# Performance work log

Measured on AMD Instinct MI355X. Metric: run time of the kernel, lower is better.

The kernel has to match this reference:

```python
import jax, jax.numpy as jnp
import numpy as np

DEPTH = 6
INPUT_DIM = 512
HIDDEN = [128, 64]
OUT_DIM = 8
BATCH = 8192
NUM_LEAVES = 2 ** DEPTH            # 64
NUM_INTERNAL = 2 ** DEPTH - 1      # 63 routing Dense(1, sigmoid) nodes


def setup_inputs() -> dict:
    key = jax.random.key(0)
    ks = jax.random.split(key, 9)
    s = lambda fan_in: 1.0 / np.sqrt(fan_in)
    return {
        "x": jax.random.normal(ks[0], (BATCH, INPUT_DIM), dtype=jnp.float32),
        # routers: one Dense(input_dim -> 1) per internal node
        "router_W": jax.random.normal(ks[1], (NUM_INTERNAL, INPUT_DIM), dtype=jnp.float32) * s(INPUT_DIM),
        "router_b": jnp.zeros((NUM_INTERNAL,), dtype=jnp.float32),
        # leaf MLPs: Dense(512->128, relu) -> Dense(128->64, relu) -> Dense(64->8, linear), one per leaf
        "W1": jax.random.normal(ks[2], (NUM_LEAVES, INPUT_DIM, HIDDEN[0]), dtype=jnp.float32) * s(INPUT_DIM),
        "b1": jnp.zeros((NUM_LEAVES, HIDDEN[0]), dtype=jnp.float32),
        "W2": jax.random.normal(ks[3], (NUM_LEAVES, HIDDEN[0], HIDDEN[1]), dtype=jnp.float32) * s(HIDDEN[0]),
        "b2": jnp.zeros((NUM_LEAVES, HIDDEN[1]), dtype=jnp.float32),
        "W3": jax.random.normal(ks[4], (NUM_LEAVES, HIDDEN[1], OUT_DIM), dtype=jnp.float32) * s(HIDDEN[1]),
        "b3": jnp.zeros((NUM_LEAVES, OUT_DIM), dtype=jnp.float32),
    }


def reference(x, router_W, router_b, W1, b1, W2, b2, W3, b3):
    B = x.shape[0]
    depth = int(np.log2(router_W.shape[0] + 1))
    # All routing probabilities in one fused GEMM: [B, num_internal]
    route = jax.nn.sigmoid(jnp.einsum('bi,ni->bn', x, router_W) + router_b)
    # Soft routing down the tree: interleave left/right child probabilities per level.
    p = jnp.ones((B, 1), dtype=x.dtype)
    offset = 0
    for level in range(depth):  # small fixed loop over tree levels
        n = 2 ** level
        d = route[:, offset:offset + n]              # P(go left) at each node in level
        p = jnp.stack([p * d, p * (1.0 - d)], axis=-1).reshape(B, 2 * n)
        offset += n
    # p: [B, num_leaves] leaf arrival probabilities (sums to 1 per row)
    # Leaf experts as batched (grouped) GEMMs over the leaf axis l.
    h = jax.nn.relu(jnp.einsum('bi,lih->blh', x, W1) + b1)   # [B, L, 128]
    h = jax.nn.relu(jnp.einsum('blh,lhk->blk', h, W2) + b2)  # [B, L, 64]
    pred = jnp.einsum('blk,lko->blo', h, W3) + b3            # [B, L, out] (linear output act)
    # Weighted mixture over leaves.
    return jnp.einsum('bl,blo->bo', p, pred)                 # [B, out]
```

## Files before the change

kernel.cpp:

```cpp
#include <hip/hip_runtime.h>
#include <hip/hip_bf16.h>


typedef _Float16 f16;
typedef _Float16 f16x8 __attribute__((ext_vector_type(8)));
typedef float    f32x4 __attribute__((ext_vector_type(4)));
typedef float    f32x16 __attribute__((ext_vector_type(16)));

#define MFMA16(a,b,c) __builtin_amdgcn_mfma_f32_16x16x32_f16((a),(b),(c),0,0,0)
#define MFMA32(a,b,c) __builtin_amdgcn_mfma_f32_32x32x16_f16((a),(b),(c),0,0,0)

typedef const __attribute__((address_space(1))) void gv_t;
typedef __attribute__((address_space(3))) void lv_t;
__device__ __forceinline__ void cp16(const void* g, char* lds_dst) {
  __builtin_amdgcn_global_load_lds((gv_t*)g, (lv_t*)lds_dst, 16, 0, 0);
}

#define WS_XH    0u
#define WS_W1F   8388608u
#define WS_W2F   16777216u
#define WS_W3F   17825792u
#define WS_RWF   17956864u
#define WS_NEED  18022400u

#define L_X   0
#define L_H1  32768
#define L_H2  41472
#define L_P   46080
#define L_TOT 50176

__global__ __launch_bounds__(256) void prep_all(
    const float* __restrict__ x, const float* __restrict__ rW,
    const float* __restrict__ W1, const float* __restrict__ W2,
    const float* __restrict__ W3,
    f16* __restrict__ xh, f16* __restrict__ w1f, f16* __restrict__ w2f,
    f16* __restrict__ w3f, f16* __restrict__ rwf) {
  __shared__ float sb[8704];
  const int bid = blockIdx.x, t = threadIdx.x;
  if (bid < 512) {
    const int l = bid >> 3, kc = bid & 7;
    const float* src = W1 + ((size_t)l * 512 + kc * 64) * 128;
#pragma unroll
    for (int i = 0; i < 32; ++i) {
      int idx = t + i * 256;
      int k_l = idx >> 7, n = idx & 127;
      sb[n * 68 + k_l] = src[(size_t)k_l * 128 + n];
    }
    __syncthreads();
#pragma unroll
    for (int p = 0; p < 4; ++p) {
      int c = p * 4 + (t >> 6);
      int ng = c >> 2, ksl = c & 3;
      int lane = t & 63;
      int n = ng * 32 + (lane & 31);
      int k0 = ksl * 16 + (lane >> 5) * 8;
      f16x8 h;
#pragma unroll
      for (int j = 0; j < 8; ++j) h[j] = (f16)sb[n * 68 + k0 + j];
      *(f16x8*)(w1f + ((size_t)((l * 4 + ng) * 32 + kc * 4 + ksl) * 64 + lane) * 8) = h;
    }
  } else if (bid < 768) {
    size_t base = (size_t)(bid - 512) * 16384;
#pragma unroll
    for (int i = 0; i < 8; ++i) {
      size_t idx = base + ((size_t)t + i * 256) * 8;
      float4 a = *(const float4*)(x + idx);
      float4 b = *(const float4*)(x + idx + 4);
      f16x8 h = {(f16)a.x,(f16)a.y,(f16)a.z,(f16)a.w,(f16)b.x,(f16)b.y,(f16)b.z,(f16)b.w};
      *(f16x8*)(xh + idx) = h;
    }
  } else if (bid < 832) {
    const int l = bid - 768;
    const float* src = W2 + (size_t)l * 128 * 64;
#pragma unroll
    for (int i = 0; i < 32; ++i) {
      int idx = t + i * 256;
      int k_l = idx >> 6, n = idx & 63;
      sb[n * 132 + k_l] = src[(size_t)k_l * 64 + n];
    }
    __syncthreads();
#pragma unroll
    for (int p = 0; p < 4; ++p) {
      int c = p * 4 + (t >> 6);
      int nb = c >> 2, ks = c & 3;
      int lane = t & 63;
      int n = nb * 16 + (lane & 15);
      int k0 = ks * 32 + (lane >> 4) * 8;
      f16x8 h;
#pragma unroll
      for (int j = 0; j < 8; ++j) h[j] = (f16)sb[n * 132 + k0 + j];
      *(f16x8*)(w2f + ((size_t)((l * 4 + nb) * 4 + ks) * 64 + lane) * 8) = h;
    }
    if (t < 128) {
      int ks = t >> 6, lane = t & 63;
      int n = lane & 15;
      int k0 = ks * 32 + (lane >> 4) * 8;
      f16x8 h;
#pragma unroll
      for (int j = 0; j < 8; ++j)
        h[j] = (n < 8) ? (f16)W3[((size_t)l * 64 + k0 + j) * 8 + n] : (f16)0.f;
      *(f16x8*)(w3f + ((size_t)(l * 2 + ks) * 64 + lane) * 8) = h;
    }
  } else {
    int c = (bid - 832) * 4 + (t >> 6);
    int ngr = c >> 5, ks = c & 31;
    int lane = t & 63;
    int n = ngr * 32 + (lane & 31);
    int k0 = ks * 16 + (lane >> 5) * 8;
    f16x8 h;
#pragma unroll
    for (int j = 0; j < 8; ++j)
      h[j] = (n < 63) ? (f16)rW[(size_t)n * 512 + k0 + j] : (f16)0.f;
    *(f16x8*)(rwf + ((size_t)c * 64 + lane) * 8) = h;
  }
}

__global__ __launch_bounds__(256, 2) void fused_tree(
    const f16* __restrict__ xh, const f16* __restrict__ w1f,
    const f16* __restrict__ w2f, const f16* __restrict__ w3f,
    const f16* __restrict__ rwf, const float* __restrict__ rb,
    const float* __restrict__ b1, const float* __restrict__ b2,
    const float* __restrict__ b3, float* __restrict__ out) {
  __shared__ char smem[L_TOT];
  f16*   x_lds   = (f16*)(smem + L_X);
  f16*   h1_lds  = (f16*)(smem + L_H1);
  float* route_s = (float*)(smem + L_H1);
  f16*   h2_lds  = (f16*)(smem + L_H2);
  float* p_lds   = (float*)(smem + L_P);

  const int t = threadIdx.x;
  const int w = t >> 6, L = t & 63;
  const int l16 = L & 15, quad = L >> 4;
  const int r31 = L & 31, kp = L >> 5;

  const int bid = blockIdx.x;
  const int r8 = bid & 7;
  const int lg0 = (r8 >> 1) * 16;
  const int btp = (bid >> 3) * 2 + (r8 & 1);
  const int b0 = btp * 64;

#pragma unroll
  for (int j = 0; j < 8; ++j) {
    int r = w * 8 + j;
    int u = (L & 56) | ((L & 7) ^ (r & 7));
    cp16(xh + (size_t)(b0 + 32 + r) * 512 + u * 8, smem + r * 1024);
  }
  f16x8 a0[32];
#pragma unroll
  for (int ks = 0; ks < 32; ++ks)
    a0[ks] = *(const f16x8*)(xh + (size_t)(b0 + r31) * 512 + ks * 16 + kp * 8);
  __syncthreads();

  {
    const int btr = w >> 1, ngr = w & 1;
    f32x16 accr;
#pragma unroll
    for (int i = 0; i < 16; ++i) accr[i] = 0.f;
    const f16* rbase = rwf + (size_t)(ngr * 32) * 512 + (size_t)L * 8;
#pragma unroll
    for (int ks = 0; ks < 32; ++ks) {
      f16x8 B = *(const f16x8*)(rbase + (size_t)ks * 512);
      f16x8 A;
      if (btr == 0) A = a0[ks];
      else {
        int u = ks * 2 + kp;
        A = *(const f16x8*)(x_lds + r31 * 512 + ((u & 56) | ((u & 7) ^ (r31 & 7))) * 8);
      }
      accr = MFMA32(A, B, accr);
    }
    int node = ngr * 32 + r31;
    float rbv = (node < 63) ? rb[node] : 0.f;
#pragma unroll
    for (int reg = 0; reg < 16; ++reg) {
      int rr = btr * 32 + (reg & 3) + 8 * (reg >> 2) + 4 * kp;
      route_s[rr * 68 + node] = 1.f / (1.f + __expf(-(accr[reg] + rbv)));
    }
  }
  __syncthreads();
  float prod[4];
  {
    int row = t >> 2, j0 = t & 3;
#pragma unroll
    for (int i = 0; i < 4; ++i) {
      int l = lg0 + j0 * 4 + i;
      float pr = 1.f;
#pragma unroll
      for (int lev = 0; lev < 6; ++lev) {
        int node = (1 << lev) - 1 + (l >> (6 - lev));
        float d = route_s[row * 68 + node];
        pr *= ((l >> (5 - lev)) & 1) ? (1.f - d) : d;
      }
      prod[i] = pr;
    }
  }
  __syncthreads();
  {
    int row = t >> 2, j0 = t & 3;
#pragma unroll
    for (int i = 0; i < 4; ++i) p_lds[row * 16 + j0 * 4 + i] = prod[i];
  }
  __syncthreads();

  const f16* w1base = w1f + ((size_t)(lg0 * 4 + w) * 32) * 512 + (size_t)L * 8;
  f16x8 bq[2][4];
#pragma unroll
  for (int s = 0; s < 4; ++s) bq[0][s] = *(const f16x8*)(w1base + (size_t)s * 512);

  f32x4 acc_out = {0.f, 0.f, 0.f, 0.f};
  const int mt = w >> 1, nt2 = w & 1;

#pragma unroll 1
  for (int li = 0; li < 16; ++li) {
    const int l = lg0 + li;
    const size_t leafoff = (size_t)li * 65536;

    f32x16 acc1r, acc1l;
#pragma unroll
    for (int i = 0; i < 16; ++i) { acc1r[i] = 0.f; acc1l[i] = 0.f; }

#pragma unroll
    for (int q = 0; q < 8; ++q) {
      size_t nxt = (q < 7) ? (leafoff + (size_t)(q + 1) * 2048)
                           : ((li < 15) ? (leafoff + 65536) : (leafoff + 7 * 2048));
#pragma unroll
      for (int s = 0; s < 4; ++s)
        bq[(q + 1) & 1][s] = *(const f16x8*)(w1base + nxt + (size_t)s * 512);
#pragma unroll
      for (int s = 0; s < 4; ++s) {
        int ks = q * 4 + s;
        int u = ks * 2 + kp;
        f16x8 A1 = *(const f16x8*)(x_lds + r31 * 512 + ((u & 56) | ((u & 7) ^ (r31 & 7))) * 8);
        acc1r = MFMA32(a0[ks], bq[q & 1][s], acc1r);
        acc1l = MFMA32(A1, bq[q & 1][s], acc1l);
      }
    }

    f16x8 bw2[2][4];
#pragma unroll
    for (int n16 = 0; n16 < 2; ++n16)
#pragma unroll
      for (int ks = 0; ks < 4; ++ks)
        bw2[n16][ks] = *(const f16x8*)(w2f + ((size_t)((l * 4 + nt2 * 2 + n16) * 4 + ks) * 64 + L) * 8);
    f16x8 bw3[2];
#pragma unroll
    for (int ks = 0; ks < 2; ++ks)
      bw3[ks] = *(const f16x8*)(w3f + ((size_t)(l * 2 + ks) * 64 + L) * 8);

    const int n1 = w * 32 + r31;
    const float bias1 = b1[l * 128 + n1];

#pragma unroll
    for (int reg = 0; reg < 16; ++reg) {
      int rr = (reg & 3) + 8 * (reg >> 2) + 4 * kp;
      float v = acc1r[reg] + bias1;
      h1_lds[rr * 136 + n1] = (f16)(v > 0.f ? v : 0.f);
    }
    __syncthreads();

#define GEMM2_BT(btv)                                                          \
    {                                                                          \
      f32x4 acc2[2] = {{0.f,0.f,0.f,0.f},{0.f,0.f,0.f,0.f}};                   \
      _Pragma("unroll")                                                        \
      for (int ks = 0; ks < 4; ++ks) {                                         \
        f16x8 A = *(const f16x8*)(h1_lds + (mt * 16 + l16) * 136 + ks * 32 + quad * 8); \
        _Pragma("unroll")                                                      \
        for (int n16 = 0; n16 < 2; ++n16) acc2[n16] = MFMA16(A, bw2[n16][ks], acc2[n16]); \
      }                                                                        \
      _Pragma("unroll")                                                        \
      for (int n16 = 0; n16 < 2; ++n16) {                                      \
        int n2 = nt2 * 32 + n16 * 16 + l16;                                    \
        float bias2 = b2[l * 64 + n2];                                         \
        _Pragma("unroll")                                                      \
        for (int rg = 0; rg < 4; ++rg) {                                       \
          int r2 = mt * 16 + quad * 4 + rg;                                    \
          float v = acc2[n16][rg] + bias2;                                     \
          v = v > 0.f ? v : 0.f;                                               \
          h2_lds[r2 * 72 + n2] = (f16)(v * p_lds[((btv) * 32 + r2) * 16 + li]); \
        }                                                                      \
      }                                                                        \
    }

    GEMM2_BT(0)
    __syncthreads();

    if (w < 2) {
#pragma unroll
      for (int ks = 0; ks < 2; ++ks) {
        f16x8 A = *(const f16x8*)(h2_lds + ((w & 1) * 16 + l16) * 72 + ks * 32 + quad * 8);
        acc_out = MFMA16(A, bw3[ks], acc_out);
      }
    }
#pragma unroll
    for (int reg = 0; reg < 16; ++reg) {
      int rr = (reg & 3) + 8 * (reg >> 2) + 4 * kp;
      float v = acc1l[reg] + bias1;
      h1_lds[rr * 136 + n1] = (f16)(v > 0.f ? v : 0.f);
    }
    __syncthreads();

    GEMM2_BT(1)
    __syncthreads();

    if (w >= 2) {
#pragma unroll
      for (int ks = 0; ks < 2; ++ks) {
        f16x8 A = *(const f16x8*)(h2_lds + ((w & 1) * 16 + l16) * 72 + ks * 32 + quad * 8);
        acc_out = MFMA16(A, bw3[ks], acc_out);
      }
    }
#undef GEMM2_BT
  }

  if (l16 < 8) {
    const int btf = w >> 1, mtf = w & 1;
    float b3v[16];
#pragma unroll
    for (int li2 = 0; li2 < 16; ++li2) b3v[li2] = b3[(lg0 + li2) * 8 + l16];
#pragma unroll
    for (int rg = 0; rg < 4; ++rg) {
      int rloc = btf * 32 + mtf * 16 + quad * 4 + rg;
      float v = acc_out[rg];
#pragma unroll
      for (int li2 = 0; li2 < 16; ++li2) v += p_lds[rloc * 16 + li2] * b3v[li2];
      atomicAdd(out + (size_t)(b0 + rloc) * 8 + l16, v);
    }
  }
}

extern "C" void kernel_launch(void* const* d_in, const int* in_sizes, int n_in,
                              void* d_out, int out_size, void* d_ws, size_t ws_size,
                              hipStream_t stream) {
  const float* x  = (const float*)d_in[0];
  const float* rW = (const float*)d_in[1];
  const float* rb = (const float*)d_in[2];
  const float* W1 = (const float*)d_in[3];
  const float* b1 = (const float*)d_in[4];
  const float* W2 = (const float*)d_in[5];
  const float* b2 = (const float*)d_in[6];
  const float* W3 = (const float*)d_in[7];
  const float* b3 = (const float*)d_in[8];
  float* out = (float*)d_out;

  if (ws_size < WS_NEED) return;

  char* ws = (char*)d_ws;
  f16* xh  = (f16*)(ws + WS_XH);
  f16* w1f = (f16*)(ws + WS_W1F);
  f16* w2f = (f16*)(ws + WS_W2F);
  f16* w3f = (f16*)(ws + WS_W3F);
  f16* rwf = (f16*)(ws + WS_RWF);

  hipMemsetAsync(d_out, 0, (size_t)out_size * sizeof(float), stream);
  prep_all<<<848, 256, 0, stream>>>(x, rW, W1, W2, W3, xh, w1f, w2f, w3f, rwf);
  fused_tree<<<512, 256, 0, stream>>>(xh, w1f, w2f, w3f, rwf, rb, b1, b2, b3, out);
}
```

Measured before the change: 207.1 us.

## Restructure per-leaf layer-2/3 to per-wave rows, cutting barriers; deepen W1 prefetch

The leaf loop now writes both 32-row halves of h1 to LDS together. Each wave then computes layer 2 for its own 16 rows across all 64 outputs and runs layer 3 from a private per-wave h2 buffer. This drops the per-leaf barriers from four to two and removes the idle-wave phases in layer 3, at the cost of more LDS and more W2 fragment registers per wave. W1 prefetch deepens to two stages, and the prep kernel is reworked to use coalesced float4 loads, transposing through shared memory with more blocks.

Result: slower. 243.7 us (+17.7%).

```diff
diff --git a/kernel.cpp b/kernel.cpp
--- a/kernel.cpp
+++ b/kernel.cpp
@@ -25,9 +25,9 @@
 
 #define L_X   0
 #define L_H1  32768
-#define L_H2  41472
-#define L_P   46080
-#define L_TOT 50176
+#define L_H2  50176
+#define L_P   59392
+#define L_TOT 63488
 
 __global__ __launch_bounds__(256) void prep_all(
     const float* __restrict__ x, const float* __restrict__ rW,
@@ -37,30 +37,30 @@
     f16* __restrict__ w3f, f16* __restrict__ rwf) {
   __shared__ float sb[8704];
   const int bid = blockIdx.x, t = threadIdx.x;
-  if (bid < 512) {
-    const int l = bid >> 3, kc = bid & 7;
-    const float* src = W1 + ((size_t)l * 512 + kc * 64) * 128;
-#pragma unroll
-    for (int i = 0; i < 32; ++i) {
-      int idx = t + i * 256;
-      int k_l = idx >> 7, n = idx & 127;
-      sb[n * 68 + k_l] = src[(size_t)k_l * 128 + n];
+  const int lane = t & 63, quad = (lane >> 4) & 3, l16 = lane & 15;
+  const int r31 = lane & 31, kp = lane >> 5;
+
+  if (bid < 1024) {
+    const int l = bid >> 4, kc32 = bid & 15;
+    const float* src = W1 + ((size_t)l * 512 + kc32 * 32) * 128;
+#pragma unroll
+    for (int i = 0; i < 4; ++i) {
+      int f4 = i * 256 + t;
+      int k = f4 >> 5, nf4 = f4 & 31;
+      *(float4*)(sb + k * 132 + nf4 * 4) = *(const float4*)(src + k * 128 + nf4 * 4);
     }
     __syncthreads();
 #pragma unroll
-    for (int p = 0; p < 4; ++p) {
-      int c = p * 4 + (t >> 6);
-      int ng = c >> 2, ksl = c & 3;
-      int lane = t & 63;
-      int n = ng * 32 + (lane & 31);
-      int k0 = ksl * 16 + (lane >> 5) * 8;
-      f16x8 h;
-#pragma unroll
-      for (int j = 0; j < 8; ++j) h[j] = (f16)sb[n * 68 + k0 + j];
-      *(f16x8*)(w1f + ((size_t)((l * 4 + ng) * 32 + kc * 4 + ksl) * 64 + lane) * 8) = h;
-    }
-  } else if (bid < 768) {
-    size_t base = (size_t)(bid - 512) * 16384;
+    for (int h = 0; h < 2; ++h) {
+      int fid = (t >> 6) + h * 4;
+      int ng = fid >> 1, hh = fid & 1;
+      f16x8 o;
+#pragma unroll
+      for (int j = 0; j < 8; ++j) o[j] = (f16)sb[(hh * 16 + kp * 8 + j) * 132 + ng * 32 + r31];
+      *(f16x8*)(w1f + ((size_t)(l * 4 + ng) * 32 + kc32 * 2 + hh) * 512 + lane * 8) = o;
+    }
+  } else if (bid < 1280) {
+    size_t base = (size_t)(bid - 1024) * 16384;
 #pragma unroll
     for (int i = 0; i < 8; ++i) {
       size_t idx = base + ((size_t)t + i * 256) * 8;
@@ -69,49 +69,42 @@
       f16x8 h = {(f16)a.x,(f16)a.y,(f16)a.z,(f16)a.w,(f16)b.x,(f16)b.y,(f16)b.z,(f16)b.w};
       *(f16x8*)(xh + idx) = h;
     }
-  } else if (bid < 832) {
-    const int l = bid - 768;
+  } else if (bid < 1344) {
+    const int l = bid - 1280;
     const float* src = W2 + (size_t)l * 128 * 64;
 #pragma unroll
-    for (int i = 0; i < 32; ++i) {
-      int idx = t + i * 256;
-      int k_l = idx >> 6, n = idx & 63;
-      sb[n * 132 + k_l] = src[(size_t)k_l * 64 + n];
+    for (int i = 0; i < 8; ++i) {
+      int f4 = i * 256 + t;
+      int k = f4 >> 4, nf4 = f4 & 15;
+      *(float4*)(sb + k * 68 + nf4 * 4) = *(const float4*)(src + k * 64 + nf4 * 4);
     }
     __syncthreads();
 #pragma unroll
-    for (int p = 0; p < 4; ++p) {
-      int c = p * 4 + (t >> 6);
-      int nb = c >> 2, ks = c & 3;
-      int lane = t & 63;
-      int n = nb * 16 + (lane & 15);
-      int k0 = ks * 32 + (lane >> 4) * 8;
-      f16x8 h;
-#pragma unroll
-      for (int j = 0; j < 8; ++j) h[j] = (f16)sb[n * 132 + k0 + j];
-      *(f16x8*)(w2f + ((size_t)((l * 4 + nb) * 4 + ks) * 64 + lane) * 8) = h;
+    for (int i = 0; i < 4; ++i) {
+      int fid = (t >> 6) + i * 4;
+      int nb = fid >> 2, ks = fid & 3;
+      f16x8 o;
+#pragma unroll
+      for (int j = 0; j < 8; ++j) o[j] = (f16)sb[(ks * 32 + quad * 8 + j) * 68 + nb * 16 + l16];
+      *(f16x8*)(w2f + ((size_t)(l * 4 + nb) * 4 + ks) * 512 + lane * 8) = o;
     }
     if (t < 128) {
-      int ks = t >> 6, lane = t & 63;
-      int n = lane & 15;
-      int k0 = ks * 32 + (lane >> 4) * 8;
-      f16x8 h;
+      int kc3 = t >> 6;
+      f16x8 o;
 #pragma unroll
       for (int j = 0; j < 8; ++j)
-        h[j] = (n < 8) ? (f16)W3[((size_t)l * 64 + k0 + j) * 8 + n] : (f16)0.f;
-      *(f16x8*)(w3f + ((size_t)(l * 2 + ks) * 64 + lane) * 8) = h;
+        o[j] = (l16 < 8) ? (f16)W3[((size_t)l * 64 + kc3 * 32 + quad * 8 + j) * 8 + l16] : (f16)0.f;
+      *(f16x8*)(w3f + ((size_t)(l * 2 + kc3)) * 512 + lane * 8) = o;
     }
   } else {
-    int c = (bid - 832) * 4 + (t >> 6);
-    int ngr = c >> 5, ks = c & 31;
-    int lane = t & 63;
-    int n = ngr * 32 + (lane & 31);
-    int k0 = ks * 16 + (lane >> 5) * 8;
-    f16x8 h;
+    int c = (bid - 1344) * 4 + (t >> 6);
+    int n = ((c >> 5) * 32) + r31;
+    int k0 = (c & 31) * 16 + kp * 8;
+    f16x8 o;
 #pragma unroll
     for (int j = 0; j < 8; ++j)
-      h[j] = (n < 63) ? (f16)rW[(size_t)n * 512 + k0 + j] : (f16)0.f;
-    *(f16x8*)(rwf + ((size_t)c * 64 + lane) * 8) = h;
+      o[j] = (n < 63) ? (f16)rW[(size_t)n * 512 + k0 + j] : (f16)0.f;
+    *(f16x8*)(rwf + (size_t)c * 512 + lane * 8) = o;
   }
 }
 
@@ -125,7 +118,6 @@
   f16*   x_lds   = (f16*)(smem + L_X);
   f16*   h1_lds  = (f16*)(smem + L_H1);
   float* route_s = (float*)(smem + L_H1);
-  f16*   h2_lds  = (f16*)(smem + L_H2);
   float* p_lds   = (float*)(smem + L_P);
 
   const int t = threadIdx.x;
@@ -136,8 +128,9 @@
   const int bid = blockIdx.x;
   const int r8 = bid & 7;
   const int lg0 = (r8 >> 1) * 16;
-  const int btp = (bid >> 3) * 2 + (r8 & 1);
-  const int b0 = btp * 64;
+  const int b0 = ((bid >> 3) * 2 + (r8 & 1)) * 64;
+
+  f16* h2w = (f16*)(smem + L_H2 + w * 2304);
 
 #pragma unroll
   for (int j = 0; j < 8; ++j) {
@@ -199,127 +192,112 @@
 #pragma unroll
     for (int i = 0; i < 4; ++i) p_lds[row * 16 + j0 * 4 + i] = prod[i];
   }
+
+  const f16* w1base = w1f + (size_t)(lg0 * 4 + w) * 32 * 512 + (size_t)L * 8;
+  f16x8 bq[4][4];
+#pragma unroll
+  for (int s = 0; s < 4; ++s) {
+    bq[0][s] = *(const f16x8*)(w1base + (size_t)s * 512);
+    bq[1][s] = *(const f16x8*)(w1base + 2048 + (size_t)s * 512);
+  }
+  f32x4 acc3 = {0.f, 0.f, 0.f, 0.f};
+  const int n1 = w * 32 + r31;
   __syncthreads();
-
-  const f16* w1base = w1f + ((size_t)(lg0 * 4 + w) * 32) * 512 + (size_t)L * 8;
-  f16x8 bq[2][4];
-#pragma unroll
-  for (int s = 0; s < 4; ++s) bq[0][s] = *(const f16x8*)(w1base + (size_t)s * 512);
-
-  f32x4 acc_out = {0.f, 0.f, 0.f, 0.f};
-  const int mt = w >> 1, nt2 = w & 1;
 
 #pragma unroll 1
   for (int li = 0; li < 16; ++li) {
     const int l = lg0 + li;
-    const size_t leafoff = (size_t)li * 65536;
 
     f32x16 acc1r, acc1l;
 #pragma unroll
     for (int i = 0; i < 16; ++i) { acc1r[i] = 0.f; acc1l[i] = 0.f; }
-
 #pragma unroll
     for (int q = 0; q < 8; ++q) {
-      size_t nxt = (q < 7) ? (leafoff + (size_t)(q + 1) * 2048)
-                           : ((li < 15) ? (leafoff + 65536) : (leafoff + 7 * 2048));
+      int g = li * 8 + q + 2;
+      if (g > 127) g = 127;
+      const f16* pre = w1base + ((size_t)(g >> 3) << 16) + (size_t)(g & 7) * 2048;
 #pragma unroll
       for (int s = 0; s < 4; ++s)
-        bq[(q + 1) & 1][s] = *(const f16x8*)(w1base + nxt + (size_t)s * 512);
+        bq[(q + 2) & 3][s] = *(const f16x8*)(pre + (size_t)s * 512);
 #pragma unroll
       for (int s = 0; s < 4; ++s) {
         int ks = q * 4 + s;
         int u = ks * 2 + kp;
         f16x8 A1 = *(const f16x8*)(x_lds + r31 * 512 + ((u & 56) | ((u & 7) ^ (r31 & 7))) * 8);
-        acc1r = MFMA32(a0[ks], bq[q & 1][s], acc1r);
-        acc1l = MFMA32(A1, bq[q & 1][s], acc1l);
-      }
-    }
-
-    f16x8 bw2[2][4];
-#pragma unroll
-    for (int n16 = 0; n16 < 2; ++n16)
+        acc1r = MFMA32(a0[ks], bq[q & 3][s], acc1r);
+        acc1l = MFMA32(A1, bq[q & 3][s], acc1l);
+      }
+    }
+
+    {
+      float bias1 = b1[l * 128 + n1];
+#pragma unroll
+      for (int reg = 0; reg < 16; ++reg) {
+        int rr = (reg & 3) + 8 * (reg >> 2) + 4 * kp;
+        float vr = acc1r[reg] + bias1;
+        float vl = acc1l[reg] + bias1;
+        h1_lds[rr * 136 + n1]        = (f16)(vr > 0.f ? vr : 0.f);
+        h1_lds[(32 + rr) * 136 + n1] = (f16)(vl > 0.f ? vl : 0.f);
+      }
+    }
+    f16x8 bw2[4][4];
+#pragma unroll
+    for (int nb = 0; nb < 4; ++nb)
 #pragma unroll
       for (int ks = 0; ks < 4; ++ks)
-        bw2[n16][ks] = *(const f16x8*)(w2f + ((size_t)((l * 4 + nt2 * 2 + n16) * 4 + ks) * 64 + L) * 8);
+        bw2[nb][ks] = *(const f16x8*)(w2f + ((size_t)(l * 4 + nb) * 4 + ks) * 512 + (size_t)L * 8);
     f16x8 bw3[2];
 #pragma unroll
-    for (int ks = 0; ks < 2; ++ks)
-      bw3[ks] = *(const f16x8*)(w3f + ((size_t)(l * 2 + ks) * 64 + L) * 8);
-
-    const int n1 = w * 32 + r31;
-    const float bias1 = b1[l * 128 + n1];
-
-#pragma unroll
-    for (int reg = 0; reg < 16; ++reg) {
-      int rr = (reg & 3) + 8 * (reg >> 2) + 4 * kp;
-      float v = acc1r[reg] + bias1;
-      h1_lds[rr * 136 + n1] = (f16)(v > 0.f ? v : 0.f);
-    }
+    for (int kc3 = 0; kc3 < 2; ++kc3)
+      bw3[kc3] = *(const f16x8*)(w3f + ((size_t)(l * 2 + kc3)) * 512 + (size_t)L * 8);
     __syncthreads();
 
-#define GEMM2_BT(btv)                                                          \
-    {                                                                          \
-      f32x4 acc2[2] = {{0.f,0.f,0.f,0.f},{0.f,0.f,0.f,0.f}};                   \
-      _Pragma("unroll")                                                        \
-      for (int ks = 0; ks < 4; ++ks) {                                         \
-        f16x8 A = *(const f16x8*)(h1_lds + (mt * 16 + l16) * 136 + ks * 32 + quad * 8); \
-        _Pragma("unroll")                                                      \
-        for (int n16 = 0; n16 < 2; ++n16) acc2[n16] = MFMA16(A, bw2[n16][ks], acc2[n16]); \
-      }                                                                        \
-      _Pragma("unroll")                                                        \
-      for (int n16 = 0; n16 < 2; ++n16) {                                      \
-        int n2 = nt2 * 32 + n16 * 16 + l16;                                    \
-        float bias2 = b2[l * 64 + n2];                                         \
-        _Pragma("unroll")                                                      \
-        for (int rg = 0; rg < 4; ++rg) {                                       \
-          int r2 = mt * 16 + quad * 4 + rg;                                    \
-          float v = acc2[n16][rg] + bias2;                                     \
-          v = v > 0.f ? v : 0.f;                                               \
-          h2_lds[r2 * 72 + n2] = (f16)(v * p_lds[((btv) * 32 + r2) * 16 + li]); \
-        }                                                                      \
-      }                                                                        \
-    }
-
-    GEMM2_BT(0)
+    f16x8 afr[4];
+#pragma unroll
+    for (int ks = 0; ks < 4; ++ks)
+      afr[ks] = *(const f16x8*)(h1_lds + (w * 16 + l16) * 136 + ks * 32 + quad * 8);
     __syncthreads();
 
-    if (w < 2) {
-#pragma unroll
-      for (int ks = 0; ks < 2; ++ks) {
-        f16x8 A = *(const f16x8*)(h2_lds + ((w & 1) * 16 + l16) * 72 + ks * 32 + quad * 8);
-        acc_out = MFMA16(A, bw3[ks], acc_out);
-      }
-    }
-#pragma unroll
-    for (int reg = 0; reg < 16; ++reg) {
-      int rr = (reg & 3) + 8 * (reg >> 2) + 4 * kp;
-      float v = acc1l[reg] + bias1;
-      h1_lds[rr * 136 + n1] = (f16)(v > 0.f ? v : 0.f);
-    }
-    __syncthreads();
-
-    GEMM2_BT(1)
-    __syncthreads();
-
-    if (w >= 2) {
-#pragma unroll
-      for (int ks = 0; ks < 2; ++ks) {
-        f16x8 A = *(const f16x8*)(h2_lds + ((w & 1) * 16 + l16) * 72 + ks * 32 + quad * 8);
-        acc_out = MFMA16(A, bw3[ks], acc_out);
-      }
-    }
-#undef GEMM2_BT
+    f32x4 acc2[4];
+#pragma unroll
+    for (int nb = 0; nb < 4; ++nb) acc2[nb] = (f32x4){0.f,0.f,0.f,0.f};
+#pragma unroll
+    for (int ks = 0; ks < 4; ++ks)
+#pragma unroll
+      for (int nb = 0; nb < 4; ++nb)
+        acc2[nb] = MFMA16(afr[ks], bw2[nb][ks], acc2[nb]);
+
+    float pv[4];
+#pragma unroll
+    for (int rg = 0; rg < 4; ++rg)
+      pv[rg] = p_lds[(w * 16 + quad * 4 + rg) * 16 + li];
+#pragma unroll
+    for (int nb = 0; nb < 4; ++nb) {
+      int n2 = nb * 16 + l16;
+      float bias2 = b2[l * 64 + n2];
+#pragma unroll
+      for (int rg = 0; rg < 4; ++rg) {
+        float v = acc2[nb][rg] + bias2;
+        v = v > 0.f ? v : 0.f;
+        h2w[(quad * 4 + rg) * 72 + n2] = (f16)(v * pv[rg]);
+      }
+    }
+
+#pragma unroll
+    for (int kc3 = 0; kc3 < 2; ++kc3) {
+      f16x8 A3 = *(const f16x8*)(h2w + l16 * 72 + kc3 * 32 + quad * 8);
+      acc3 = MFMA16(A3, bw3[kc3], acc3);
+    }
   }
 
   if (l16 < 8) {
-    const int btf = w >> 1, mtf = w & 1;
     float b3v[16];
 #pragma unroll
     for (int li2 = 0; li2 < 16; ++li2) b3v[li2] = b3[(lg0 + li2) * 8 + l16];
 #pragma unroll
     for (int rg = 0; rg < 4; ++rg) {
-      int rloc = btf * 32 + mtf * 16 + quad * 4 + rg;
-      float v = acc_out[rg];
+      int rloc = w * 16 + quad * 4 + rg;
+      float v = acc3[rg];
 #pragma unroll
       for (int li2 = 0; li2 < 16; ++li2) v += p_lds[rloc * 16 + li2] * b3v[li2];
       atomicAdd(out + (size_t)(b0 + rloc) * 8 + l16, v);
@@ -351,6 +329,6 @@
   f16* rwf = (f16*)(ws + WS_RWF);
 
   hipMemsetAsync(d_out, 0, (size_t)out_size * sizeof(float), stream);
-  prep_all<<<848, 256, 0, stream>>>(x, rW, W1, W2, W3, xh, w1f, w2f, w3f, rwf);
+  prep_all<<<1360, 256, 0, stream>>>(x, rW, W1, W2, W3, xh, w1f, w2f, w3f, rwf);
   fused_tree<<<512, 256, 0, stream>>>(xh, w1f, w2f, w3f, rwf, rb, b1, b2, b3, out);
 }
```
